# Kernel tuning notes

Hardware: AMD Instinct MI355X
Metric: run time of the kernel (lower is better)

Reference implementation:

```python
import jax, jax.numpy as jnp
import numpy as np

FREQ_THRESHOLD = 0.1


def setup_inputs() -> dict:
    key = jax.random.key(0)
    images = jax.random.uniform(key, (32, 3, 512, 512), dtype=jnp.float32)
    return {"images": images}


def reference(images):
    # images: [B, C, H, W]
    B, C, H, W = images.shape
    gray = jnp.mean(images, axis=1)                      # [B, H, W]
    fft_magnitude = jnp.abs(jnp.fft.fft2(gray))          # [B, H, W]

    # Radial low-frequency mask centered at (H//2, W//2) -- computed once,
    # shared across the batch (replaces the per-pixel Python loop).
    center_h, center_w = H // 2, W // 2
    radius = min(H, W) * FREQ_THRESHOLD
    yy = jnp.arange(H, dtype=jnp.float32)[:, None]
    xx = jnp.arange(W, dtype=jnp.float32)[None, :]
    dist = jnp.sqrt((yy - center_h) ** 2 + (xx - center_w) ** 2)
    low_freq_mask = (dist <= radius).astype(fft_magnitude.dtype)  # [H, W]

    low_freq_energy = jnp.sum(fft_magnitude * low_freq_mask, axis=(1, 2))  # [B]
    total_energy = jnp.sum(fft_magnitude, axis=(1, 2))                     # [B]
    mura_scores = low_freq_energy / total_energy                           # [B]
    return jnp.mean(mura_scores)                                           # scalar
```

## Files before the change

### kernel.cpp

```cpp
#include <hip/hip_runtime.h>
#include <math.h>

#define N 512
#define NPAD(i) ((i) + ((i) >> 5))
#define FSZ 532
#define NCOL 257
#define RAD2 2621.44f
#define SQ2H 0.70710678f

__device__ __forceinline__ void dft8(float (&xr)[8], float (&xi)[8]) {
    float e0r = xr[0] + xr[4], e0i = xi[0] + xi[4];
    float e1r = xr[0] - xr[4], e1i = xi[0] - xi[4];
    float e2r = xr[2] + xr[6], e2i = xi[2] + xi[6];
    float e3r = xr[2] - xr[6], e3i = xi[2] - xi[6];
    float E0r = e0r + e2r, E0i = e0i + e2i;
    float E2r = e0r - e2r, E2i = e0i - e2i;
    float E1r = e1r + e3i, E1i = e1i - e3r;
    float E3r = e1r - e3i, E3i = e1i + e3r;
    float o0r = xr[1] + xr[5], o0i = xi[1] + xi[5];
    float o1r = xr[1] - xr[5], o1i = xi[1] - xi[5];
    float o2r = xr[3] + xr[7], o2i = xi[3] + xi[7];
    float o3r = xr[3] - xr[7], o3i = xi[3] - xi[7];
    float O0r = o0r + o2r, O0i = o0i + o2i;
    float O2r = o0r - o2r, O2i = o0i - o2i;
    float O1r = o1r + o3i, O1i = o1i - o3r;
    float O3r = o1r - o3i, O3i = o1i + o3r;
    float t1r = SQ2H * (O1r + O1i), t1i = SQ2H * (O1i - O1r);
    float t2r = O2i,                t2i = -O2r;
    float t3r = SQ2H * (O3i - O3r), t3i = -SQ2H * (O3r + O3i);
    xr[0] = E0r + O0r; xi[0] = E0i + O0i;
    xr[4] = E0r - O0r; xi[4] = E0i - O0i;
    xr[1] = E1r + t1r; xi[1] = E1i + t1i;
    xr[5] = E1r - t1r; xi[5] = E1i - t1i;
    xr[2] = E2r + t2r; xi[2] = E2i + t2i;
    xr[6] = E2r - t2r; xi[6] = E2i - t2i;
    xr[3] = E3r + t3r; xi[3] = E3i + t3i;
    xr[7] = E3r - t3r; xi[7] = E3i - t3i;
}

__device__ __forceinline__ void fft512_x2(float (&ar)[8], float (&ai)[8],
                                          float (&br)[8], float (&bi)[8],
                                          int l) {
#pragma unroll
    for (int half = 32; half >= 1; half >>= 1) {
        const int j = l & (half - 1);
        const float f = (float)j * (0.5f / (float)half);
        const float c = __builtin_amdgcn_cosf(f);
        const float s = __builtin_amdgcn_sinf(f);
        const bool up = (l & half) != 0;
        const float sgn = up ? -1.0f : 1.0f;
        const float wc  = up ? c : 1.0f;
        const float ws  = up ? s : 0.0f;
#pragma unroll
        for (int k = 0; k < 8; ++k) {
            float pr = __shfl_xor(ar[k], half);
            float pi = __shfl_xor(ai[k], half);
            float qr = __shfl_xor(br[k], half);
            float qi = __shfl_xor(bi[k], half);
            float tr = fmaf(sgn, ar[k], pr);
            float ti = fmaf(sgn, ai[k], pi);
            float ur = fmaf(sgn, br[k], qr);
            float ui = fmaf(sgn, bi[k], qi);
            ar[k] = tr * wc + ti * ws;
            ai[k] = ti * wc - tr * ws;
            br[k] = ur * wc + ui * ws;
            bi[k] = ui * wc - ur * ws;
        }
    }
    const int w = __brev((unsigned)l) >> 26;
#pragma unroll
    for (int k = 1; k < 8; ++k) {
        const float f = (float)(k * w) * (1.0f / 512.0f);
        const float c = __builtin_amdgcn_cosf(f);
        const float s = __builtin_amdgcn_sinf(f);
        float tr = ar[k] * c + ai[k] * s;
        float ti = ai[k] * c - ar[k] * s;
        ar[k] = tr; ai[k] = ti;
        float ur = br[k] * c + bi[k] * s;
        float ui = bi[k] * c - br[k] * s;
        br[k] = ur; bi[k] = ui;
    }
    dft8(ar, ai);
    dft8(br, bi);
}

__global__ __launch_bounds__(512) void k_gray_rowfft(
    const float* __restrict__ img, float2* __restrict__ buf) {
    __shared__ float sr[16][FSZ], si[16][FSZ];
    const int t = threadIdx.x, wv = t >> 6, l = t & 63;
    const int b = blockIdx.y, tile = blockIdx.x;
    const size_t plane = (size_t)N * N;
    const float* base = img + (size_t)b * 3 * plane;
    const int r0 = tile * 32 + 4 * wv;

    const float inv3 = 1.0f / 3.0f;
    auto loadgray = [&](const float* p, float (&g)[8]) {
        const float4* c0 = (const float4*)p;
        const float4* c1 = (const float4*)(p + plane);
        const float4* c2 = (const float4*)(p + 2 * plane);
#pragma unroll
        for (int q = 0; q < 2; ++q) {
            float4 a = c0[2 * l + q], bb = c1[2 * l + q], c = c2[2 * l + q];
            g[4 * q + 0] = (a.x + bb.x + c.x) * inv3;
            g[4 * q + 1] = (a.y + bb.y + c.y) * inv3;
            g[4 * q + 2] = (a.z + bb.z + c.z) * inv3;
            g[4 * q + 3] = (a.w + bb.w + c.w) * inv3;
        }
    };

    float arr[8], ari[8], brr[8], bri[8];
    loadgray(base + (size_t)(r0 + 0) * N, arr);
    loadgray(base + (size_t)(r0 + 1) * N, ari);
    loadgray(base + (size_t)(r0 + 2) * N, brr);
    loadgray(base + (size_t)(r0 + 3) * N, bri);

    fft512_x2(arr, ari, brr, bri, l);

    const int w = __brev((unsigned)l) >> 26;
    const int sA = 2 * wv, sB = 2 * wv + 1;
#pragma unroll
    for (int k = 0; k < 8; ++k) {
        int u = w + 64 * k;
        sr[sA][NPAD(u)] = arr[k]; si[sA][NPAD(u)] = ari[k];
        sr[sB][NPAD(u)] = brr[k]; si[sB][NPAD(u)] = bri[k];
    }
    __syncthreads();

    const int p = t & 15;
    const int h2 = 2 * p;
    const int slot = t >> 4;
    float2* ob = buf + (size_t)b * NCOL * N;
#pragma unroll
    for (int it = 0; it < 9; ++it) {
        int v = slot + 32 * it;
        if (v < NCOL) {
            int vn = (N - v) & (N - 1);
            float Zr  = sr[p][NPAD(v)],  Zi  = si[p][NPAD(v)];
            float Zr2 = sr[p][NPAD(vn)], Zi2 = si[p][NPAD(vn)];
            float4 o;
            o.x = 0.5f * (Zr + Zr2);
            o.y = 0.5f * (Zi - Zi2);
            o.z = 0.5f * (Zi + Zi2);
            o.w = 0.5f * (Zr2 - Zr);
            *(float4*)(&ob[(size_t)v * N + tile * 32 + h2]) = o;
        }
    }
}

__global__ __launch_bounds__(256) void k_colfft_reduce(
    const float2* __restrict__ buf, float* __restrict__ acc) {
    __shared__ float red[8];
    const int t = threadIdx.x, wv = t >> 6, l = t & 63;
    const int b = blockIdx.y;
    const int v0 = blockIdx.x * 8 + 2 * wv;
    const int v1 = v0 + 1;
    const int c0 = v0 > 256 ? 256 : v0;
    const int c1 = v1 > 256 ? 256 : v1;

    const float4* colA = (const float4*)(buf + ((size_t)b * NCOL + c0) * N);
    const float4* colB = (const float4*)(buf + ((size_t)b * NCOL + c1) * N);
    float arr[8], ari[8], brr[8], bri[8];
#pragma unroll
    for (int q = 0; q < 4; ++q) {
        float4 zA = colA[4 * l + q];
        float4 zB = colB[4 * l + q];
        arr[2 * q] = zA.x; ari[2 * q] = zA.y;
        arr[2 * q + 1] = zA.z; ari[2 * q + 1] = zA.w;
        brr[2 * q] = zB.x; bri[2 * q] = zB.y;
        brr[2 * q + 1] = zB.z; bri[2 * q + 1] = zB.w;
    }

    fft512_x2(arr, ari, brr, bri, l);

    const float wA = (v0 == 0 || v0 == 256) ? 1.0f : (v0 < 256 ? 2.0f : 0.0f);
    const float wB = (v1 == 0 || v1 == 256) ? 1.0f : (v1 < 256 ? 2.0f : 0.0f);
    const float dxA = (float)(c0 - 256), dxA2 = dxA * dxA;
    const float dxB = (float)(c1 - 256), dxB2 = dxB * dxB;
    const int w = __brev((unsigned)l) >> 26;
    float msum = 0.0f, tsum = 0.0f;
#pragma unroll
    for (int k = 0; k < 8; ++k) {
        int u = w + 64 * k;
        float dy = (float)(u - 256);
        float dy2 = dy * dy;
        float magA = sqrtf(arr[k] * arr[k] + ari[k] * ari[k]) * wA;
        float magB = sqrtf(brr[k] * brr[k] + bri[k] * bri[k]) * wB;
        tsum += magA + magB;
        float m = 0.0f;
        if (dy2 + dxA2 <= RAD2) m += magA;
        if (dy2 + dxB2 <= RAD2) m += magB;
        msum += m;
    }
#pragma unroll
    for (int off = 32; off > 0; off >>= 1) {
        msum += __shfl_down(msum, off);
        tsum += __shfl_down(tsum, off);
    }
    if (l == 0) { red[wv * 2] = msum; red[wv * 2 + 1] = tsum; }
    __syncthreads();
    if (t == 0) {
        atomicAdd(&acc[b * 2 + 0], red[0] + red[2] + red[4] + red[6]);
        atomicAdd(&acc[b * 2 + 1], red[1] + red[3] + red[5] + red[7]);
    }
}

__global__ void k_final(const float* __restrict__ acc,
                        float* __restrict__ out) {
    int t = threadIdx.x;
    float r = 0.0f;
    if (t < 32) r = acc[t * 2 + 0] / acc[t * 2 + 1];
#pragma unroll
    for (int off = 32; off > 0; off >>= 1) r += __shfl_down(r, off);
    if (t == 0) out[0] = r * (1.0f / 32.0f);
}

extern "C" void kernel_launch(void* const* d_in, const int* in_sizes, int n_in,
                              void* d_out, int out_size, void* d_ws,
                              size_t ws_size, hipStream_t stream) {
    const float* img = (const float*)d_in[0];
    float* out = (float*)d_out;

    float2* buf = (float2*)d_ws;
    const size_t buf_bytes = (size_t)32 * NCOL * N * sizeof(float2);
    float* acc = (float*)((char*)d_ws + buf_bytes);

    hipMemsetAsync(acc, 0, 64 * sizeof(float), stream);

    dim3 g1(N / 32, 32);
    k_gray_rowfft<<<g1, 512, 0, stream>>>(img, buf);

    dim3 g2((NCOL + 7) / 8, 32);
    k_colfft_reduce<<<g2, 256, 0, stream>>>(buf, acc);

    k_final<<<1, 64, 0, stream>>>(acc, out);
}
```

Measured before the change: 175.9 us.

## Replace shuffle-based column FFT with radix-8 LDS three-pass FFT

The column FFT kernel now does one 512-point column per wavefront instead of two. It uses a three-stage radix-8 decomposition (8x8x8) that exchanges data through per-wave shared memory, in place of six stages of cross-lane shuffles. The goal is to cut the heavy shuffle traffic and twiddle computation of the butterfly-by-shuffle approach. In exchange it adds LDS round trips, doubles the number of blocks, and gives each thread less independent work, which may lower ILP.

```diff
diff --git a/kernel.cpp b/kernel.cpp
--- a/kernel.cpp
+++ b/kernel.cpp
@@ -149,48 +149,81 @@
 
 __global__ __launch_bounds__(256) void k_colfft_reduce(
     const float2* __restrict__ buf, float* __restrict__ acc) {
+    __shared__ float2 lds[4][528];
     __shared__ float red[8];
     const int t = threadIdx.x, wv = t >> 6, l = t & 63;
     const int b = blockIdx.y;
-    const int v0 = blockIdx.x * 8 + 2 * wv;
-    const int v1 = v0 + 1;
-    const int c0 = v0 > 256 ? 256 : v0;
-    const int c1 = v1 > 256 ? 256 : v1;
-
-    const float4* colA = (const float4*)(buf + ((size_t)b * NCOL + c0) * N);
-    const float4* colB = (const float4*)(buf + ((size_t)b * NCOL + c1) * N);
-    float arr[8], ari[8], brr[8], bri[8];
-#pragma unroll
-    for (int q = 0; q < 4; ++q) {
-        float4 zA = colA[4 * l + q];
-        float4 zB = colB[4 * l + q];
-        arr[2 * q] = zA.x; ari[2 * q] = zA.y;
-        arr[2 * q + 1] = zA.z; ari[2 * q + 1] = zA.w;
-        brr[2 * q] = zB.x; bri[2 * q] = zB.y;
-        brr[2 * q + 1] = zB.z; bri[2 * q + 1] = zB.w;
-    }
-
-    fft512_x2(arr, ari, brr, bri, l);
-
-    const float wA = (v0 == 0 || v0 == 256) ? 1.0f : (v0 < 256 ? 2.0f : 0.0f);
-    const float wB = (v1 == 0 || v1 == 256) ? 1.0f : (v1 < 256 ? 2.0f : 0.0f);
-    const float dxA = (float)(c0 - 256), dxA2 = dxA * dxA;
-    const float dxB = (float)(c1 - 256), dxB2 = dxB * dxB;
-    const int w = __brev((unsigned)l) >> 26;
+    const int v = blockIdx.x * 4 + wv;
+    const int vv = v > 256 ? 256 : v;
+
+    const float2* col = buf + ((size_t)b * NCOL + vv) * N;
+    float2* W = lds[wv];
+
+    float xr[8], xi[8];
+#pragma unroll
+    for (int a = 0; a < 8; ++a) {
+        float2 z = col[64 * a + l];
+        xr[a] = z.x; xi[a] = z.y;
+    }
+
+    dft8(xr, xi);
+    const int bb = l >> 3, cc = l & 7;
+#pragma unroll
+    for (int k0 = 1; k0 < 8; ++k0) {
+        const float f = (float)(bb * k0) * (1.0f / 64.0f);
+        const float c = __builtin_amdgcn_cosf(f);
+        const float s = __builtin_amdgcn_sinf(f);
+        float tr = xr[k0] * c + xi[k0] * s;
+        float ti = xi[k0] * c - xr[k0] * s;
+        xr[k0] = tr; xi[k0] = ti;
+    }
+#pragma unroll
+    for (int k0 = 0; k0 < 8; ++k0)
+        W[66 * k0 + l] = make_float2(xr[k0], xi[k0]);
+    __builtin_amdgcn_wave_barrier();
+#pragma unroll
+    for (int bq = 0; bq < 8; ++bq) {
+        float2 z = W[66 * bb + 8 * bq + cc];
+        xr[bq] = z.x; xi[bq] = z.y;
+    }
+
+    dft8(xr, xi);
+#pragma unroll
+    for (int k1 = 0; k1 < 8; ++k1) {
+        const int e = cc * (bb + 8 * k1);
+        const float f = (float)e * (1.0f / 512.0f);
+        const float c = __builtin_amdgcn_cosf(f);
+        const float s = __builtin_amdgcn_sinf(f);
+        float tr = xr[k1] * c + xi[k1] * s;
+        float ti = xi[k1] * c - xr[k1] * s;
+        xr[k1] = tr; xi[k1] = ti;
+    }
+    __builtin_amdgcn_wave_barrier();
+#pragma unroll
+    for (int k1 = 0; k1 < 8; ++k1)
+        W[66 * k1 + l] = make_float2(xr[k1], xi[k1]);
+    __builtin_amdgcn_wave_barrier();
+#pragma unroll
+    for (int c2 = 0; c2 < 8; ++c2) {
+        float2 z = W[66 * (l >> 3) + 8 * (l & 7) + c2];
+        xr[c2] = z.x; xi[c2] = z.y;
+    }
+
+    dft8(xr, xi);
+
+    const float wcol = (v == 0 || v == 256) ? 1.0f : (v < 256 ? 2.0f : 0.0f);
+    const float dx = (float)(vv - 256);
+    const float dx2 = dx * dx;
     float msum = 0.0f, tsum = 0.0f;
 #pragma unroll
-    for (int k = 0; k < 8; ++k) {
-        int u = w + 64 * k;
+    for (int k2 = 0; k2 < 8; ++k2) {
+        int u = l + 64 * k2;
+        float mag = sqrtf(xr[k2] * xr[k2] + xi[k2] * xi[k2]);
+        tsum += mag;
         float dy = (float)(u - 256);
-        float dy2 = dy * dy;
-        float magA = sqrtf(arr[k] * arr[k] + ari[k] * ari[k]) * wA;
-        float magB = sqrtf(brr[k] * brr[k] + bri[k] * bri[k]) * wB;
-        tsum += magA + magB;
-        float m = 0.0f;
-        if (dy2 + dxA2 <= RAD2) m += magA;
-        if (dy2 + dxB2 <= RAD2) m += magB;
-        msum += m;
-    }
+        if (dy * dy + dx2 <= RAD2) msum += mag;
+    }
+    msum *= wcol; tsum *= wcol;
 #pragma unroll
     for (int off = 32; off > 0; off >>= 1) {
         msum += __shfl_down(msum, off);
@@ -229,7 +262,7 @@
     dim3 g1(N / 32, 32);
     k_gray_rowfft<<<g1, 512, 0, stream>>>(img, buf);
 
-    dim3 g2((NCOL + 7) / 8, 32);
+    dim3 g2((NCOL + 3) / 4, 32);
     k_colfft_reduce<<<g2, 256, 0, stream>>>(buf, acc);
 
     k_final<<<1, 64, 0, stream>>>(acc, out);
```

Result: slower. 186.6 us (+6.1%).
